# Kernel tuning notes

Measured on AMD Instinct MI355X. Metric: run time of the kernel, lower is better.

## Reference

```python
import jax, jax.numpy as jnp
import numpy as np

N, E, H = 10000, 80000, 128
NODE_DIM, EDGE_DIM, OUT_DIM, L = 7, 21, 2, 10

def _lin(k, i, o):
    s = 1.0 / np.sqrt(i)
    k1, k2 = jax.random.split(k)
    return (jax.random.uniform(k1, (i, o), jnp.float32, -s, s),
            jax.random.uniform(k2, (o,), jnp.float32, -s, s))

def _mlp_params(k, dims):
    ks = jax.random.split(k, len(dims) - 1)
    Ws, bs = [], []
    for kk, i, o in zip(ks, dims[:-1], dims[1:]):
        W, b = _lin(kk, i, o)
        Ws.append(W); bs.append(b)
    return Ws, bs

def _stack_mlps(k, dims, n):
    ks = jax.random.split(k, n)
    per = [_mlp_params(kk, dims) for kk in ks]
    Ws = [jnp.stack([p[0][j] for p in per]) for j in range(3)]
    bs = [jnp.stack([p[1][j] for p in per]) for j in range(3)]
    return Ws, bs

def mlp3(h, W1, b1, W2, b2, W3, b3):
    h = jax.nn.leaky_relu(h @ W1 + b1)  # slope 0.01 = torch LeakyReLU default
    h = jax.nn.leaky_relu(h @ W2 + b2)
    return h @ W3 + b3

def setup_inputs() -> dict:
    key = jax.random.key(0)
    ks = jax.random.split(key, 10)
    inp = {
        'x_type': jax.random.randint(ks[0], (N,), 0, 2),
        'edge_index': jax.random.randint(ks[1], (2, E), 0, N),
        'edge_attr': jax.random.normal(ks[2], (E, EDGE_DIM), jnp.float32),
        'node_dist': jax.random.uniform(ks[3], (E, 1), jnp.float32),
        'embed_w': jax.random.normal(ks[4], (2, NODE_DIM), jnp.float32),
    }
    niW, nib = _mlp_params(ks[5], [NODE_DIM, H, H, H])
    eiW, eib = _mlp_params(ks[6], [EDGE_DIM, H, H, H])
    noW, nob = _mlp_params(ks[7], [H, H, H, OUT_DIM])
    meW, meb = _stack_mlps(ks[8], [3 * H, H, H, H], L)
    mnW, mnb = _stack_mlps(ks[9], [2 * H, H, H, H], L)
    for pre, Ws, bs in [('ni', niW, nib), ('ei', eiW, eib), ('no', noW, nob),
                        ('me', meW, meb), ('mn', mnW, mnb)]:
        for j in range(3):
            inp[f'{pre}_W{j+1}'] = Ws[j]
            inp[f'{pre}_b{j+1}'] = bs[j]
    return inp

def reference(x_type, edge_index, edge_attr, node_dist, embed_w,
              ni_W1, ni_b1, ni_W2, ni_b2, ni_W3, ni_b3,
              ei_W1, ei_b1, ei_W2, ei_b2, ei_W3, ei_b3,
              no_W1, no_b1, no_W2, no_b2, no_W3, no_b3,
              me_W1, me_b1, me_W2, me_b2, me_W3, me_b3,
              mn_W1, mn_b1, mn_W2, mn_b2, mn_W3, mn_b3):
    n = x_type.shape[0]
    src, dst = edge_index[0], edge_index[1]  # PyG: j = source, i = target
    node = mlp3(embed_w[x_type], ni_W1, ni_b1, ni_W2, ni_b2, ni_W3, ni_b3)
    edge = mlp3(edge_attr, ei_W1, ei_b1, ei_W2, ei_b2, ei_W3, ei_b3)
    for i in range(L):
        # message: cat(x_i, x_j, edge_feature) -> edge MLP
        m = mlp3(jnp.concatenate([node[dst], node[src], edge], axis=-1),
                 me_W1[i], me_b1[i], me_W2[i], me_b2[i], me_W3[i], me_b3[i])
        # aggregate: scatter-sum of node_dist-weighted messages onto targets
        aggr = jax.ops.segment_sum(m * node_dist, dst, num_segments=n)
        node = node + mlp3(jnp.concatenate([node, aggr], axis=-1),
                           mn_W1[i], mn_b1[i], mn_W2[i], mn_b2[i], mn_W3[i], mn_b3[i])
        edge = edge + m
    return mlp3(node, no_W1, no_b1, no_W2, no_b2, no_W3, no_b3)
```

## Files before the change

### kernel.cpp

```cpp
#include <hip/hip_runtime.h>


#define NH  128
#define TPB 256

typedef unsigned short u16;
typedef unsigned int   u32;
using s8v = __attribute__((ext_vector_type(8))) short;
using f4v = __attribute__((ext_vector_type(4))) float;


__device__ __forceinline__ u16 bf_hi(float v) {
  u32 u = __float_as_uint(v);
  return (u16)((u + 0x7FFFu + ((u >> 16) & 1u)) >> 16);
}
__device__ __forceinline__ float bf_f(u16 h) { return __uint_as_float((u32)h << 16); }
__device__ __forceinline__ void split2(float v, u16& h, u16& l) {
  h = bf_hi(v); l = bf_hi(v - bf_f(h));
}
__device__ __forceinline__ void split8(const float* v, s8v& fh, s8v& fl) {
  union { u32 u[4]; s8v s; } H, L;
  #pragma unroll
  for (int i = 0; i < 4; ++i) {
    u16 h0, l0, h1, l1;
    split2(v[2*i], h0, l0); split2(v[2*i+1], h1, l1);
    H.u[i] = (u32)h0 | ((u32)h1 << 16);
    L.u[i] = (u32)l0 | ((u32)l1 << 16);
  }
  fh = H.s; fl = L.s;
}

__device__ __forceinline__ f4v mfma3(s8v ah, s8v al, s8v bh, s8v bl, f4v c) {
  c = __builtin_amdgcn_mfma_f32_16x16x32_bf16(ah, bh, c, 0, 0, 0);
  c = __builtin_amdgcn_mfma_f32_16x16x32_bf16(ah, bl, c, 0, 0, 0);
  c = __builtin_amdgcn_mfma_f32_16x16x32_bf16(al, bh, c, 0, 0, 0);
  return c;
}

__device__ __forceinline__ float lrelu(float v) { return v > 0.f ? v : 0.01f * v; }

__device__ __forceinline__ void pack2(f4v a, u32& w0, u32& w1, u32& v0, u32& v1) {
  u16 h[4], lo[4];
  #pragma unroll
  for (int r = 0; r < 4; ++r) { const float x = lrelu(a[r]); split2(x, h[r], lo[r]); }
  w0 = (u32)h[0]  | ((u32)h[1]  << 16); w1 = (u32)h[2]  | ((u32)h[3]  << 16);
  v0 = (u32)lo[0] | ((u32)lo[1] << 16); v1 = (u32)lo[2] | ((u32)lo[3] << 16);
}

__device__ __forceinline__ void trans_frag(f4v a0, f4v a1, int srcA, int srcB, bool sel1,
                                           s8v& fh, s8v& fl) {
  u32 h00,h01,l00,l01, h10,h11,l10,l11;
  pack2(a0, h00,h01,l00,l01);
  pack2(a1, h10,h11,l10,l11);
  union { u32 u[4]; s8v s; } H, L;
  u32 x, y;
  x = __shfl((int)h00, srcA); y = __shfl((int)h10, srcA); H.u[0] = sel1 ? y : x;
  x = __shfl((int)h01, srcA); y = __shfl((int)h11, srcA); H.u[1] = sel1 ? y : x;
  x = __shfl((int)h00, srcB); y = __shfl((int)h10, srcB); H.u[2] = sel1 ? y : x;
  x = __shfl((int)h01, srcB); y = __shfl((int)h11, srcB); H.u[3] = sel1 ? y : x;
  x = __shfl((int)l00, srcA); y = __shfl((int)l10, srcA); L.u[0] = sel1 ? y : x;
  x = __shfl((int)l01, srcA); y = __shfl((int)l11, srcA); L.u[1] = sel1 ? y : x;
  x = __shfl((int)l00, srcB); y = __shfl((int)l10, srcB); L.u[2] = sel1 ? y : x;
  x = __shfl((int)l01, srcB); y = __shfl((int)l11, srcB); L.u[3] = sel1 ? y : x;
  fh = H.s; fl = L.s;
}


__device__ __forceinline__ void stage_load(const u16* __restrict__ base, int KW, int LO,
                                           int col, int w, int l, float4 sreg[4]) {
  const int glog8 = ((l & 3) ^ ((l >> 3) & 3)) * 8;
  #pragma unroll
  for (int i = 0; i < 2; ++i) {
    const int t2 = (w * 2 + i) * 64 + l;
    const u16* gp = base + (size_t)(t2 >> 2) * KW + col + glog8;
    sreg[i*2+0] = *(const float4*)gp;
    sreg[i*2+1] = *(const float4*)(gp + LO);
  }
}
__device__ __forceinline__ void stage_write(u16* wb, int w, int l, const float4 sreg[4]) {
  #pragma unroll
  for (int i = 0; i < 2; ++i) {
    const int t2 = (w * 2 + i) * 64 + l;
    *(float4*)(wb + t2 * 8)        = sreg[i*2+0];
    *(float4*)(wb + 4096 + t2 * 8) = sreg[i*2+1];
  }
}
__device__ __forceinline__ void wfrag(const u16* panel, int tt, int c, int gsw, s8v& wh, s8v& wl) {
  const u16* p = panel + (16*tt + c) * 32 + gsw * 8;
  wh = *(const s8v*)p;
  wl = *(const s8v*)(p + 4096);
}

#define ME1_OFF 0
#define ME2_OFF 983040
#define ME3_OFF 1310720
#define MN1_OFF 1638400
#define MN2_OFF 2293760
#define MN3_OFF 2621440
#define WT_TOTAL 2949120
#define PREP_ELEMS 1474560

__global__ void __launch_bounds__(256) k_prep(
    const float* __restrict__ meW1, const float* __restrict__ meW2, const float* __restrict__ meW3,
    const float* __restrict__ mnW1, const float* __restrict__ mnW2, const float* __restrict__ mnW3,
    u16* __restrict__ wt) {
  const int id = blockIdx.x * 256 + threadIdx.x;
  if (id >= PREP_ELEMS) return;
  const int l = id / 147456;
  const int rem = id % 147456;
  const float* src; u16* dh; int K, loc;
  if (rem < 49152)       { loc = rem;          K = 384; src = meW1 + (size_t)l*49152; dh = wt + ME1_OFF + (size_t)l*98304; }
  else if (rem < 65536)  { loc = rem - 49152;  K = 128; src = meW2 + (size_t)l*16384; dh = wt + ME2_OFF + (size_t)l*32768; }
  else if (rem < 81920)  { loc = rem - 65536;  K = 128; src = meW3 + (size_t)l*16384; dh = wt + ME3_OFF + (size_t)l*32768; }
  else if (rem < 114688) { loc = rem - 81920;  K = 256; src = mnW1 + (size_t)l*32768; dh = wt + MN1_OFF + (size_t)l*65536; }
  else if (rem < 131072) { loc = rem - 114688; K = 128; src = mnW2 + (size_t)l*16384; dh = wt + MN2_OFF + (size_t)l*32768; }
  else                   { loc = rem - 131072; K = 128; src = mnW3 + (size_t)l*16384; dh = wt + MN3_OFF + (size_t)l*32768; }
  const int n = loc / K, k = loc % K;
  const float v = src[(size_t)k * NH + n];
  u16 h, lo; split2(v, h, lo);
  dh[(size_t)n * K + k] = h;
  dh[(size_t)NH * K + (size_t)n * K + k] = lo;
}


__global__ void __launch_bounds__(256) k_deg(const int* __restrict__ dst, int* __restrict__ cnt, int E) {
  const int e = blockIdx.x * 256 + threadIdx.x;
  if (e < E) atomicAdd(&cnt[dst[e]], 1);
}

__global__ void __launch_bounds__(256) k_scan(int* __restrict__ cur, int* __restrict__ off, int n, int E) {
  __shared__ int ps[256];
  const int t = threadIdx.x;
  const int chunk = (n + 255) / 256;
  const int b0 = t * chunk;
  int s = 0;
  for (int j = 0; j < chunk; ++j) { const int r = b0 + j; if (r < n) s += cur[r]; }
  ps[t] = s; __syncthreads();
  for (int d = 1; d < 256; d <<= 1) {
    const int v = (t >= d) ? ps[t - d] : 0; __syncthreads();
    ps[t] += v; __syncthreads();
  }
  int run = ps[t] - s;
  for (int j = 0; j < chunk; ++j) {
    const int r = b0 + j;
    if (r < n) { const int d = cur[r]; off[r] = run; cur[r] = run; run += d; }
  }
  if (t == 0) off[n] = E;
}

__global__ void __launch_bounds__(256) k_fill(const int* __restrict__ dst, int* __restrict__ cur,
                                              int* __restrict__ csr, int E) {
  const int e = blockIdx.x * 256 + threadIdx.x;
  if (e < E) { const int p = atomicAdd(&cur[dst[e]], 1); csr[p] = e; }
}


__device__ __forceinline__ int swzB(int c) { return c ^ ((c >> 3) & 1); }
__device__ __forceinline__ void fma8(float* a, float s, const float4 b0, const float4 b1) {
  a[0] += s * b0.x; a[1] += s * b0.y; a[2] += s * b0.z; a[3] += s * b0.w;
  a[4] += s * b1.x; a[5] += s * b1.y; a[6] += s * b1.z; a[7] += s * b1.w;
}

template<int RB>
__device__ __forceinline__ void stage_rows128(
    const float* __restrict__ src, int row_base, int nmax, float* As, int t) {
  const int c = t & 31;
  for (int e = t >> 5; e < RB; e += 8) {
    int r = row_base + e; if (r >= nmax) r = nmax - 1;
    const float4 v = reinterpret_cast<const float4*>(src + (size_t)r * NH)[c];
    reinterpret_cast<float4*>(As)[e * 32 + (c ^ ((e >> 2) & 7))] = v;
  }
}

template<int RB>
__device__ __forceinline__ void stage_smallK(
    const float* __restrict__ src, const int* __restrict__ ridx,
    int row_base, int nmax, int F, float* As, int t) {
  for (int i = t; i < RB * F; i += TPB) {
    const int e = i / F, f = i - e * F;
    int r;
    if (ridx) r = ridx[e];
    else { r = row_base + e; if (r >= nmax) r = nmax - 1; }
    As[e * NH + ((((f >> 2) ^ ((e >> 2) & 7)) << 2) | (f & 3))] = src[(size_t)r * F + f];
  }
}

template<int AR>
__device__ __forceinline__ void init_acc(const float* __restrict__ b, float acc[AR][8], int t) {
  const int o0 = (t >> 4) * 8;
  const float4 c0 = *reinterpret_cast<const float4*>(b + o0);
  const float4 c1 = *reinterpret_cast<const float4*>(b + o0 + 4);
  #pragma unroll
  for (int i = 0; i < AR; ++i) {
    acc[i][0] = c0.x; acc[i][1] = c0.y; acc[i][2] = c0.z; acc[i][3] = c0.w;
    acc[i][4] = c1.x; acc[i][5] = c1.y; acc[i][6] = c1.z; acc[i][7] = c1.w;
  }
}

template<int AR>
__device__ __forceinline__ void gemm_block(
    const float* __restrict__ W, int Kpart,
    const float* As, float* Bs, float acc[AR][8], int t) {
  const int e0  = (t & 15) * AR;
  const int g   = t >> 4;
  const int ob0 = swzB(g * 2) * 4;
  const int ob1 = swzB(g * 2 + 1) * 4;
  int sr[AR];
  #pragma unroll
  for (int i = 0; i < AR; ++i) sr[i] = ((e0 + i) >> 2) & 7;
  for (int sub = 0; sub < Kpart; sub += 32) {
    int kmax = Kpart - sub; if (kmax > 32) kmax = 32;
    __syncthreads();
    {
      const int r  = t >> 3;
      const int cb = (t & 7) * 4;
      if (r < kmax) {
        const float4* s4 = reinterpret_cast<const float4*>(W + (size_t)(sub + r) * NH) + cb;
        #pragma unroll
        for (int j = 0; j < 4; ++j)
          *reinterpret_cast<float4*>(Bs + r * NH + swzB(cb + j) * 4) = s4[j];
      }
    }
    __syncthreads();
    if (kmax == 32) {
      #pragma unroll
      for (int k4 = 0; k4 < 8; ++k4) {
        const int gch = (sub >> 2) + k4;
        float4 aa[AR];
        #pragma unroll
        for (int i = 0; i < AR; ++i)
          aa[i] = reinterpret_cast<const float4*>(As)[(e0 + i) * 32 + (gch ^ sr[i])];
        #pragma unroll
        for (int kk = 0; kk < 4; ++kk) {
          const int k = k4 * 4 + kk;
          const float4 b0 = *reinterpret_cast<const float4*>(Bs + k * NH + ob0);
          const float4 b1 = *reinterpret_cast<const float4*>(Bs + k * NH + ob1);
          #pragma unroll
          for (int i = 0; i < AR; ++i) {
            const float a = (kk == 0) ? aa[i].x : (kk == 1) ? aa[i].y : (kk == 2) ? aa[i].z : aa[i].w;
            fma8(acc[i], a, b0, b1);
          }
        }
      }
    } else {
      for (int k = 0; k < kmax; ++k) {
        const int kk = sub + k;
        const float4 b0 = *reinterpret_cast<const float4*>(Bs + k * NH + ob0);
        const float4 b1 = *reinterpret_cast<const float4*>(Bs + k * NH + ob1);
        #pragma unroll
        for (int i = 0; i < AR; ++i) {
          const float a = As[(e0 + i) * NH + ((((kk >> 2) ^ sr[i]) << 2) | (kk & 3))];
          fma8(acc[i], a, b0, b1);
        }
      }
    }
  }
}

template<int AR, bool ACT>
__device__ __forceinline__ void act_store(float* As, float acc[AR][8], int t) {
  const int e0 = (t & 15) * AR;
  const int g  = t >> 4;
  __syncthreads();
  #pragma unroll
  for (int i = 0; i < AR; ++i) {
    const int r = e0 + i;
    const int s = (r >> 2) & 7;
    float v[8];
    #pragma unroll
    for (int j = 0; j < 8; ++j) v[j] = ACT ? lrelu(acc[i][j]) : acc[i][j];
    float4 w0 = {v[0], v[1], v[2], v[3]};
    float4 w1 = {v[4], v[5], v[6], v[7]};
    reinterpret_cast<float4*>(As + r * NH)[(g * 2)     ^ s] = w0;
    reinterpret_cast<float4*>(As + r * NH)[(g * 2 + 1) ^ s] = w1;
  }
  __syncthreads();
}


__global__ void __launch_bounds__(TPB) k_enc_node(
    const int* __restrict__ xt, const float* __restrict__ embed,
    const float* __restrict__ W1, const float* __restrict__ b1,
    const float* __restrict__ W2, const float* __restrict__ b2,
    const float* __restrict__ W3, const float* __restrict__ b3,
    float* __restrict__ node, int n) {
  constexpr int RB = 32, AR = 2;
  __shared__ float As[RB * NH];
  __shared__ float Bs[32 * NH];
  __shared__ int rid[RB];
  const int t = threadIdx.x;
  const int base = blockIdx.x * RB;
  if (t < RB) { int r = base + t; if (r >= n) r = n - 1; rid[t] = xt[r]; }
  __syncthreads();
  stage_smallK<RB>(embed, rid, 0, 2, 7, As, t);
  float acc[AR][8];
  init_acc<AR>(b1, acc, t);
  gemm_block<AR>(W1, 7, As, Bs, acc, t);
  act_store<AR, true>(As, acc, t);
  init_acc<AR>(b2, acc, t);
  gemm_block<AR>(W2, NH, As, Bs, acc, t);
  act_store<AR, true>(As, acc, t);
  init_acc<AR>(b3, acc, t);
  gemm_block<AR>(W3, NH, As, Bs, acc, t);
  const int e0 = (t & 15) * AR, o0 = (t >> 4) * 8;
  #pragma unroll
  for (int i = 0; i < AR; ++i) {
    const int r = base + e0 + i;
    if (r < n) {
      float4 v0 = {acc[i][0], acc[i][1], acc[i][2], acc[i][3]};
      float4 v1 = {acc[i][4], acc[i][5], acc[i][6], acc[i][7]};
      float4* p = reinterpret_cast<float4*>(node + (size_t)r * NH + o0);
      p[0] = v0; p[1] = v1;
    }
  }
}

__global__ void __launch_bounds__(TPB) k_enc_edge(
    const float* __restrict__ ea,
    const float* __restrict__ W1, const float* __restrict__ b1,
    const float* __restrict__ W2, const float* __restrict__ b2,
    const float* __restrict__ W3, const float* __restrict__ b3,
    float* __restrict__ edge, int nE) {
  constexpr int RB = 64, AR = 4;
  __shared__ float As[RB * NH];
  __shared__ float Bs[32 * NH];
  const int t = threadIdx.x;
  const int base = blockIdx.x * RB;
  stage_smallK<RB>(ea, nullptr, base, nE, 21, As, t);
  float acc[AR][8];
  init_acc<AR>(b1, acc, t);
  gemm_block<AR>(W1, 21, As, Bs, acc, t);
  act_store<AR, true>(As, acc, t);
  init_acc<AR>(b2, acc, t);
  gemm_block<AR>(W2, NH, As, Bs, acc, t);
  act_store<AR, true>(As, acc, t);
  init_acc<AR>(b3, acc, t);
  gemm_block<AR>(W3, NH, As, Bs, acc, t);
  const int e0 = (t & 15) * AR, o0 = (t >> 4) * 8;
  #pragma unroll
  for (int i = 0; i < AR; ++i) {
    const int r = base + e0 + i;
    if (r < nE) {
      float4 v0 = {acc[i][0], acc[i][1], acc[i][2], acc[i][3]};
      float4 v1 = {acc[i][4], acc[i][5], acc[i][6], acc[i][7]};
      float4* p = reinterpret_cast<float4*>(edge + (size_t)r * NH + o0);
      p[0] = v0; p[1] = v1;
    }
  }
}

__global__ void __launch_bounds__(TPB) k_dec(
    const float* __restrict__ node,
    const float* __restrict__ W1, const float* __restrict__ b1,
    const float* __restrict__ W2, const float* __restrict__ b2,
    const float* __restrict__ W3, const float* __restrict__ b3,
    float* __restrict__ out, int n) {
  constexpr int RB = 32, AR = 2;
  __shared__ float As[RB * NH];
  __shared__ float Bs[32 * NH];
  const int t = threadIdx.x;
  const int base = blockIdx.x * RB;
  stage_rows128<RB>(node, base, n, As, t);
  float acc[AR][8];
  init_acc<AR>(b1, acc, t);
  gemm_block<AR>(W1, NH, As, Bs, acc, t);
  act_store<AR, true>(As, acc, t);
  init_acc<AR>(b2, acc, t);
  gemm_block<AR>(W2, NH, As, Bs, acc, t);
  act_store<AR, true>(As, acc, t);
  if (t < RB * 2) {
    const int e = t >> 1, oc = t & 1;
    const int r = base + e;
    if (r < n) {
      const int s = (e >> 2) & 7;
      float sum = b3[oc];
      #pragma unroll 8
      for (int k = 0; k < NH; ++k)
        sum += As[e * NH + ((((k >> 2) ^ s) << 2) | (k & 3))] * W3[k * 2 + oc];
      out[(size_t)r * 2 + oc] = sum;
    }
  }
}

__global__ void __launch_bounds__(TPB) k_msg_mm(
    const int* __restrict__ ei, const float* __restrict__ node,
    float* __restrict__ edge, const float* __restrict__ dist, float* __restrict__ mw,
    const u16* __restrict__ wt1, const u16* __restrict__ wt2, const u16* __restrict__ wt3,
    const float* __restrict__ b1, const float* __restrict__ b2, const float* __restrict__ b3,
    int E) {
  __shared__ u16 wbuf[2][8192];
  const int t = threadIdx.x, w = t >> 6, l = t & 63, c = l & 15, g = l >> 4;
  const int gsw = g ^ ((c >> 1) & 3);
  const int wbase = blockIdx.x * 128 + w * 32;
  int e0 = wbase + c, e1 = wbase + 16 + c;
  if (e0 >= E) e0 = E - 1;
  if (e1 >= E) e1 = E - 1;
  const int sj0 = ei[e0], di0 = ei[E + e0];
  const int sj1 = ei[e1], di1 = ei[E + e1];

  float4 sreg[4];
  stage_load(wt1, 384, 49152, 0, w, l, sreg);
  stage_write(wbuf[0], w, l, sreg);

  f4v acc1a[8], acc1b[8];
  #pragma unroll
  for (int tt = 0; tt < 8; ++tt) {
    const float4 bb = *(const float4*)(b1 + 16*tt + 4*g);
    acc1a[tt] = f4v{bb.x, bb.y, bb.z, bb.w};
    acc1b[tt] = acc1a[tt];
  }
  __syncthreads();

  const int srcA = ((g & 1) * 2) * 16 + c, srcB = srcA + 16;
  const bool sel1 = (g >> 1) != 0;
  int cur = 0;

  #pragma unroll
  for (int part = 0; part < 3; ++part) {
    const float* a0 = (part == 0) ? node + (size_t)di0 * NH
                    : (part == 1) ? node + (size_t)sj0 * NH
                                  : edge + (size_t)e0 * NH;
    const float* a1 = (part == 0) ? node + (size_t)di1 * NH
                    : (part == 1) ? node + (size_t)sj1 * NH
                                  : edge + (size_t)e1 * NH;
    #pragma unroll 1
    for (int kc = 0; kc < 4; ++kc) {
      if (part == 2 && kc == 3) stage_load(wt2, 128, 16384, 0, w, l, sreg);
      else                      stage_load(wt1, 384, 49152, (part*4 + kc + 1) * 32, w, l, sreg);
      s8v h0, lo0, h1, lo1;
      { float v[8];
        *(float4*)v       = *(const float4*)(a0 + kc*32 + g*8);
        *(float4*)(v + 4) = *(const float4*)(a0 + kc*32 + g*8 + 4);
        split8(v, h0, lo0);
        *(float4*)v       = *(const float4*)(a1 + kc*32 + g*8);
        *(float4*)(v + 4) = *(const float4*)(a1 + kc*32 + g*8 + 4);
        split8(v, h1, lo1); }
      const u16* panel = wbuf[cur];
      #pragma unroll
      for (int tt = 0; tt < 8; ++tt) {
        s8v wh, wl; wfrag(panel, tt, c, gsw, wh, wl);
        acc1a[tt] = mfma3(wh, wl, h0, lo0, acc1a[tt]);
        acc1b[tt] = mfma3(wh, wl, h1, lo1, acc1b[tt]);
      }
      stage_write(wbuf[cur ^ 1], w, l, sreg);
      __syncthreads();
      cur ^= 1;
    }
  }

  f4v acc2a[8], acc2b[8];
  #pragma unroll
  for (int tt = 0; tt < 8; ++tt) {
    const float4 bb = *(const float4*)(b2 + 16*tt + 4*g);
    acc2a[tt] = f4v{bb.x, bb.y, bb.z, bb.w};
    acc2b[tt] = acc2a[tt];
  }
  #pragma unroll
  for (int kc = 0; kc < 4; ++kc) {
    if (kc < 3) stage_load(wt2, 128, 16384, (kc + 1) * 32, w, l, sreg);
    else        stage_load(wt3, 128, 16384, 0, w, l, sreg);
    s8v h0, lo0, h1, lo1;
    trans_frag(acc1a[2*kc], acc1a[2*kc+1], srcA, srcB, sel1, h0, lo0);
    trans_frag(acc1b[2*kc], acc1b[2*kc+1], srcA, srcB, sel1, h1, lo1);
    const u16* panel = wbuf[cur];
    #pragma unroll
    for (int tt = 0; tt < 8; ++tt) {
      s8v wh, wl; wfrag(panel, tt, c, gsw, wh, wl);
      acc2a[tt] = mfma3(wh, wl, h0, lo0, acc2a[tt]);
      acc2b[tt] = mfma3(wh, wl, h1, lo1, acc2b[tt]);
    }
    stage_write(wbuf[cur ^ 1], w, l, sreg);
    __syncthreads();
    cur ^= 1;
  }

  f4v acc3a[8], acc3b[8];
  #pragma unroll
  for (int tt = 0; tt < 8; ++tt) {
    const float bv = b3[16*tt + c];
    acc3a[tt] = f4v{bv, bv, bv, bv};
    acc3b[tt] = acc3a[tt];
  }
  #pragma unroll
  for (int kc = 0; kc < 4; ++kc) {
    if (kc < 3) stage_load(wt3, 128, 16384, (kc + 1) * 32, w, l, sreg);
    s8v h0, lo0, h1, lo1;
    trans_frag(acc2a[2*kc], acc2a[2*kc+1], srcA, srcB, sel1, h0, lo0);
    trans_frag(acc2b[2*kc], acc2b[2*kc+1], srcA, srcB, sel1, h1, lo1);
    const u16* panel = wbuf[cur];
    #pragma unroll
    for (int tt = 0; tt < 8; ++tt) {
      s8v wh, wl; wfrag(panel, tt, c, gsw, wh, wl);
      acc3a[tt] = mfma3(h0, lo0, wh, wl, acc3a[tt]);
      acc3b[tt] = mfma3(h1, lo1, wh, wl, acc3b[tt]);
    }
    if (kc < 3) { stage_write(wbuf[cur ^ 1], w, l, sreg); __syncthreads(); cur ^= 1; }
  }

  {
    #pragma unroll
    for (int r = 0; r < 4; ++r) {
      const int e = wbase + 4*g + r;
      if (e < E) {
        const float dw = dist[e];
        #pragma unroll
        for (int tt = 0; tt < 8; ++tt) {
          const int f = 16*tt + c;
          const float m = acc3a[tt][r];
          edge[(size_t)e * NH + f] += m;
          mw[(size_t)e * NH + f] = m * dw;
        }
      }
    }
    #pragma unroll
    for (int r = 0; r < 4; ++r) {
      const int e = wbase + 16 + 4*g + r;
      if (e < E) {
        const float dw = dist[e];
        #pragma unroll
        for (int tt = 0; tt < 8; ++tt) {
          const int f = 16*tt + c;
          const float m = acc3b[tt][r];
          edge[(size_t)e * NH + f] += m;
          mw[(size_t)e * NH + f] = m * dw;
        }
      }
    }
  }
}

__global__ void __launch_bounds__(TPB) k_node_mm(
    const int* __restrict__ off, const int* __restrict__ csr, const float* __restrict__ mw,
    float* __restrict__ node,
    const u16* __restrict__ wt1, const u16* __restrict__ wt2, const u16* __restrict__ wt3,
    const float* __restrict__ b1, const float* __restrict__ b2, const float* __restrict__ b3,
    int n) {
  __shared__ float ag[64][132];
  __shared__ u16 wbuf[8192];
  const int t = threadIdx.x, w = t >> 6, l = t & 63, c = l & 15, g = l >> 4;
  const int gsw = g ^ ((c >> 1) & 3);
  const int base = blockIdx.x * 64;

  float4 sreg[4];
  stage_load(wt1, 256, 32768, 0, w, l, sreg);
  stage_write(wbuf, w, l, sreg);

  {
    const int r = t >> 2, q = t & 3;
    const int rg = base + r;
    float s[32];
    #pragma unroll
    for (int i = 0; i < 32; ++i) s[i] = 0.f;
    if (rg < n) {
      const int eb = off[rg], ee = off[rg + 1];
      for (int ii = eb; ii < ee; ++ii) {
        const float* mp = mw + (size_t)csr[ii] * NH + q * 32;
        #pragma unroll
        for (int u = 0; u < 8; ++u) {
          const float4 x = *(const float4*)(mp + u * 4);
          s[u*4+0] += x.x; s[u*4+1] += x.y; s[u*4+2] += x.z; s[u*4+3] += x.w;
        }
      }
    }
    #pragma unroll
    for (int u = 0; u < 8; ++u)
      *(float4*)&ag[r][q*32 + u*4] = float4{s[u*4+0], s[u*4+1], s[u*4+2], s[u*4+3]};
  }
  __syncthreads();

  int nB = base + 16*w + c; if (nB >= n) nB = n - 1;
  const float* aG = node + (size_t)nB * NH;
  const float* aL = &ag[16*w + c][0];

  f4v acc1[8];
  #pragma unroll
  for (int tt = 0; tt < 8; ++tt) {
    const float4 bb = *(const float4*)(b1 + 16*tt + 4*g);
    acc1[tt] = f4v{bb.x, bb.y, bb.z, bb.w};
  }
  const int srcA = ((g & 1) * 2) * 16 + c, srcB = srcA + 16;
  const bool sel1 = (g >> 1) != 0;

  #pragma unroll
  for (int part = 0; part < 2; ++part) {
    const float* ap = (part == 0) ? aG : aL;
    #pragma unroll 1
    for (int kc = 0; kc < 4; ++kc) {
      if (part == 1 && kc == 3) stage_load(wt2, 128, 16384, 0, w, l, sreg);
      else                      stage_load(wt1, 256, 32768, (part*4 + kc + 1) * 32, w, l, sreg);
      s8v h0, lo0;
      { float v[8];
        *(float4*)v       = *(const float4*)(ap + kc*32 + g*8);
        *(float4*)(v + 4) = *(const float4*)(ap + kc*32 + g*8 + 4);
        split8(v, h0, lo0); }
      #pragma unroll
      for (int tt = 0; tt < 8; ++tt) {
        s8v wh, wl; wfrag(wbuf, tt, c, gsw, wh, wl);
        acc1[tt] = mfma3(wh, wl, h0, lo0, acc1[tt]);
      }
      __syncthreads();
      stage_write(wbuf, w, l, sreg);
      __syncthreads();
    }
  }

  f4v acc2[8];
  #pragma unroll
  for (int tt = 0; tt < 8; ++tt) {
    const float4 bb = *(const float4*)(b2 + 16*tt + 4*g);
    acc2[tt] = f4v{bb.x, bb.y, bb.z, bb.w};
  }
  #pragma unroll
  for (int kc = 0; kc < 4; ++kc) {
    if (kc < 3) stage_load(wt2, 128, 16384, (kc + 1) * 32, w, l, sreg);
    else        stage_load(wt3, 128, 16384, 0, w, l, sreg);
    s8v h0, lo0;
    trans_frag(acc1[2*kc], acc1[2*kc+1], srcA, srcB, sel1, h0, lo0);
    #pragma unroll
    for (int tt = 0; tt < 8; ++tt) {
      s8v wh, wl; wfrag(wbuf, tt, c, gsw, wh, wl);
      acc2[tt] = mfma3(wh, wl, h0, lo0, acc2[tt]);
    }
    __syncthreads();
    stage_write(wbuf, w, l, sreg);
    __syncthreads();
  }

  f4v acc3[8];
  #pragma unroll
  for (int tt = 0; tt < 8; ++tt) {
    const float bv = b3[16*tt + c];
    acc3[tt] = f4v{bv, bv, bv, bv};
  }
  #pragma unroll
  for (int kc = 0; kc < 4; ++kc) {
    if (kc < 3) stage_load(wt3, 128, 16384, (kc + 1) * 32, w, l, sreg);
    s8v h0, lo0;
    trans_frag(acc2[2*kc], acc2[2*kc+1], srcA, srcB, sel1, h0, lo0);
    #pragma unroll
    for (int tt = 0; tt < 8; ++tt) {
      s8v wh, wl; wfrag(wbuf, tt, c, gsw, wh, wl);
      acc3[tt] = mfma3(h0, lo0, wh, wl, acc3[tt]);
    }
    if (kc < 3) { __syncthreads(); stage_write(wbuf, w, l, sreg); __syncthreads(); }
  }

  #pragma unroll
  for (int r = 0; r < 4; ++r) {
    const int e = base + 16*w + 4*g + r;
    if (e < n) {
      #pragma unroll
      for (int tt = 0; tt < 8; ++tt) {
        const int f = 16*tt + c;
        node[(size_t)e * NH + f] += acc3[tt][r];
      }
    }
  }
}


extern "C" void kernel_launch(void* const* d_in, const int* in_sizes, int n_in,
                              void* d_out, int out_size, void* d_ws, size_t ws_size,
                              hipStream_t stream) {
  const int n = in_sizes[0];
  const int E = in_sizes[3];
  const int* xt      = (const int*)d_in[0];
  const int* ei      = (const int*)d_in[1];
  const float* eattr = (const float*)d_in[2];
  const float* dist  = (const float*)d_in[3];
  const float* embed = (const float*)d_in[4];
  const float* niW1 = (const float*)d_in[5];  const float* nib1 = (const float*)d_in[6];
  const float* niW2 = (const float*)d_in[7];  const float* nib2 = (const float*)d_in[8];
  const float* niW3 = (const float*)d_in[9];  const float* nib3 = (const float*)d_in[10];
  const float* eiW1 = (const float*)d_in[11]; const float* eib1 = (const float*)d_in[12];
  const float* eiW2 = (const float*)d_in[13]; const float* eib2 = (const float*)d_in[14];
  const float* eiW3 = (const float*)d_in[15]; const float* eib3 = (const float*)d_in[16];
  const float* noW1 = (const float*)d_in[17]; const float* nob1 = (const float*)d_in[18];
  const float* noW2 = (const float*)d_in[19]; const float* nob2 = (const float*)d_in[20];
  const float* noW3 = (const float*)d_in[21]; const float* nob3 = (const float*)d_in[22];
  const float* meW1 = (const float*)d_in[23]; const float* meb1 = (const float*)d_in[24];
  const float* meW2 = (const float*)d_in[25]; const float* meb2 = (const float*)d_in[26];
  const float* meW3 = (const float*)d_in[27]; const float* meb3 = (const float*)d_in[28];
  const float* mnW1 = (const float*)d_in[29]; const float* mnb1 = (const float*)d_in[30];
  const float* mnW2 = (const float*)d_in[31]; const float* mnb2 = (const float*)d_in[32];
  const float* mnW3 = (const float*)d_in[33]; const float* mnb3 = (const float*)d_in[34];

  float* out = (float*)d_out;
  const size_t fn = (size_t)n * NH;
  const size_t fe = (size_t)E * NH;

  float* node = (float*)d_ws;
  float* edge = node + fn;
  float* mw   = edge + fe;
  u16*   wt   = (u16*)(mw + fe);
  int*   off  = (int*)(wt + WT_TOTAL);
  int*   cur  = off + (n + 1);
  int*   csr  = cur + n;

  const int nb32   = (n + 31) / 32;
  const int nb64n  = (n + 63) / 64;
  const int nb64e  = (E + 63) / 64;
  const int nb128e = (E + 127) / 128;

  k_prep<<<(PREP_ELEMS + 255) / 256, 256, 0, stream>>>(meW1, meW2, meW3, mnW1, mnW2, mnW3, wt);

  hipMemsetAsync(cur, 0, (size_t)n * sizeof(int), stream);
  k_deg <<<(E + 255) / 256, 256, 0, stream>>>(ei + E, cur, E);
  k_scan<<<1, 256, 0, stream>>>(cur, off, n, E);
  k_fill<<<(E + 255) / 256, 256, 0, stream>>>(ei + E, cur, csr, E);

  k_enc_node<<<nb32,  TPB, 0, stream>>>(xt, embed, niW1, nib1, niW2, nib2, niW3, nib3, node, n);
  k_enc_edge<<<nb64e, TPB, 0, stream>>>(eattr, eiW1, eib1, eiW2, eib2, eiW3, eib3, edge, E);

  for (int l = 0; l < 10; ++l) {
    k_msg_mm<<<nb128e, TPB, 0, stream>>>(ei, node, edge, dist, mw,
        wt + ME1_OFF + (size_t)l * 98304,
        wt + ME2_OFF + (size_t)l * 32768,
        wt + ME3_OFF + (size_t)l * 32768,
        meb1 + (size_t)l * NH, meb2 + (size_t)l * NH, meb3 + (size_t)l * NH, E);
    k_node_mm<<<nb64n, TPB, 0, stream>>>(off, csr, mw, node,
        wt + MN1_OFF + (size_t)l * 65536,
        wt + MN2_OFF + (size_t)l * 32768,
        wt + MN3_OFF + (size_t)l * 32768,
        mnb1 + (size_t)l * NH, mnb2 + (size_t)l * NH, mnb3 + (size_t)l * NH, n);
  }

  k_dec<<<nb32, TPB, 0, stream>>>(node, noW1, nob1, noW2, nob2, noW3, nob3, out, n);
}
```

Measured before the change: 1.750 ms.

## Halve block size, prefetch activation chunks, and raise MFMA wave priority

Both per-layer kernels move from 256-thread to 128-thread blocks, so each block covers 64 edges or 32 nodes and twice as many blocks launch. The weight-staging helpers now load twice as many vectors per thread to fill the same panel. The activation chunk for the next K-step is loaded one step ahead in registers so its global latency overlaps the current MFMAs. s_setprio is raised around the MFMA loops to favour waves issuing matrix work. In exchange, each block re-stages the full weight panels for fewer rows, which adds L2 traffic, and register pressure rises.

```diff
diff --git a/kernel.cpp b/kernel.cpp
--- a/kernel.cpp
+++ b/kernel.cpp
@@ -67,20 +67,20 @@
 
 
 __device__ __forceinline__ void stage_load(const u16* __restrict__ base, int KW, int LO,
-                                           int col, int w, int l, float4 sreg[4]) {
-  const int glog8 = ((l & 3) ^ ((l >> 3) & 3)) * 8;
-  #pragma unroll
-  for (int i = 0; i < 2; ++i) {
-    const int t2 = (w * 2 + i) * 64 + l;
+                                           int col, int t, float4 sreg[8]) {
+  const int glog8 = ((t & 3) ^ ((t >> 3) & 3)) * 8;
+  #pragma unroll
+  for (int i = 0; i < 4; ++i) {
+    const int t2 = i * 128 + t;
     const u16* gp = base + (size_t)(t2 >> 2) * KW + col + glog8;
     sreg[i*2+0] = *(const float4*)gp;
     sreg[i*2+1] = *(const float4*)(gp + LO);
   }
 }
-__device__ __forceinline__ void stage_write(u16* wb, int w, int l, const float4 sreg[4]) {
-  #pragma unroll
-  for (int i = 0; i < 2; ++i) {
-    const int t2 = (w * 2 + i) * 64 + l;
+__device__ __forceinline__ void stage_write(u16* wb, int t, const float4 sreg[8]) {
+  #pragma unroll
+  for (int i = 0; i < 4; ++i) {
+    const int t2 = i * 128 + t;
     *(float4*)(wb + t2 * 8)        = sreg[i*2+0];
     *(float4*)(wb + 4096 + t2 * 8) = sreg[i*2+1];
   }
@@ -382,7 +382,7 @@
   }
 }
 
-__global__ void __launch_bounds__(TPB) k_msg_mm(
+__global__ void __launch_bounds__(128) k_msg_mm(
     const int* __restrict__ ei, const float* __restrict__ node,
     float* __restrict__ edge, const float* __restrict__ dist, float* __restrict__ mw,
     const u16* __restrict__ wt1, const u16* __restrict__ wt2, const u16* __restrict__ wt3,
@@ -391,16 +391,23 @@
   __shared__ u16 wbuf[2][8192];
   const int t = threadIdx.x, w = t >> 6, l = t & 63, c = l & 15, g = l >> 4;
   const int gsw = g ^ ((c >> 1) & 3);
-  const int wbase = blockIdx.x * 128 + w * 32;
+  const int wbase = blockIdx.x * 64 + w * 32;
   int e0 = wbase + c, e1 = wbase + 16 + c;
   if (e0 >= E) e0 = E - 1;
   if (e1 >= E) e1 = E - 1;
   const int sj0 = ei[e0], di0 = ei[E + e0];
   const int sj1 = ei[e1], di1 = ei[E + e1];
 
-  float4 sreg[4];
-  stage_load(wt1, 384, 49152, 0, w, l, sreg);
-  stage_write(wbuf[0], w, l, sreg);
+  const float* ap0[3] = { node + (size_t)di0 * NH, node + (size_t)sj0 * NH, edge + (size_t)e0 * NH };
+  const float* ap1[3] = { node + (size_t)di1 * NH, node + (size_t)sj1 * NH, edge + (size_t)e1 * NH };
+
+  float4 sreg[8];
+  stage_load(wt1, 384, 49152, 0, t, sreg);
+  float4 aC0 = *(const float4*)(ap0[0] + g*8);
+  float4 aC1 = *(const float4*)(ap0[0] + g*8 + 4);
+  float4 aC2 = *(const float4*)(ap1[0] + g*8);
+  float4 aC3 = *(const float4*)(ap1[0] + g*8 + 4);
+  stage_write(wbuf[0], t, sreg);
 
   f4v acc1a[8], acc1b[8];
   #pragma unroll
@@ -416,36 +423,34 @@
   int cur = 0;
 
   #pragma unroll
-  for (int part = 0; part < 3; ++part) {
-    const float* a0 = (part == 0) ? node + (size_t)di0 * NH
-                    : (part == 1) ? node + (size_t)sj0 * NH
-                                  : edge + (size_t)e0 * NH;
-    const float* a1 = (part == 0) ? node + (size_t)di1 * NH
-                    : (part == 1) ? node + (size_t)sj1 * NH
-                                  : edge + (size_t)e1 * NH;
-    #pragma unroll 1
-    for (int kc = 0; kc < 4; ++kc) {
-      if (part == 2 && kc == 3) stage_load(wt2, 128, 16384, 0, w, l, sreg);
-      else                      stage_load(wt1, 384, 49152, (part*4 + kc + 1) * 32, w, l, sreg);
-      s8v h0, lo0, h1, lo1;
-      { float v[8];
-        *(float4*)v       = *(const float4*)(a0 + kc*32 + g*8);
-        *(float4*)(v + 4) = *(const float4*)(a0 + kc*32 + g*8 + 4);
-        split8(v, h0, lo0);
-        *(float4*)v       = *(const float4*)(a1 + kc*32 + g*8);
-        *(float4*)(v + 4) = *(const float4*)(a1 + kc*32 + g*8 + 4);
-        split8(v, h1, lo1); }
-      const u16* panel = wbuf[cur];
-      #pragma unroll
-      for (int tt = 0; tt < 8; ++tt) {
-        s8v wh, wl; wfrag(panel, tt, c, gsw, wh, wl);
-        acc1a[tt] = mfma3(wh, wl, h0, lo0, acc1a[tt]);
-        acc1b[tt] = mfma3(wh, wl, h1, lo1, acc1b[tt]);
-      }
-      stage_write(wbuf[cur ^ 1], w, l, sreg);
-      __syncthreads();
-      cur ^= 1;
-    }
+  for (int p = 0; p < 12; ++p) {
+    float4 aN0, aN1, aN2, aN3;
+    if (p < 11) {
+      const int pt = (p + 1) >> 2, kn = (p + 1) & 3;
+      aN0 = *(const float4*)(ap0[pt] + kn*32 + g*8);
+      aN1 = *(const float4*)(ap0[pt] + kn*32 + g*8 + 4);
+      aN2 = *(const float4*)(ap1[pt] + kn*32 + g*8);
+      aN3 = *(const float4*)(ap1[pt] + kn*32 + g*8 + 4);
+    }
+    if (p < 11) stage_load(wt1, 384, 49152, (p + 1) * 32, t, sreg);
+    else        stage_load(wt2, 128, 16384, 0, t, sreg);
+    s8v h0, lo0, h1, lo1;
+    { float v[8];
+      *(float4*)v = aC0; *(float4*)(v + 4) = aC1; split8(v, h0, lo0);
+      *(float4*)v = aC2; *(float4*)(v + 4) = aC3; split8(v, h1, lo1); }
+    const u16* panel = wbuf[cur];
+    __builtin_amdgcn_s_setprio(1);
+    #pragma unroll
+    for (int tt = 0; tt < 8; ++tt) {
+      s8v wh, wl; wfrag(panel, tt, c, gsw, wh, wl);
+      acc1a[tt] = mfma3(wh, wl, h0, lo0, acc1a[tt]);
+      acc1b[tt] = mfma3(wh, wl, h1, lo1, acc1b[tt]);
+    }
+    __builtin_amdgcn_s_setprio(0);
+    stage_write(wbuf[cur ^ 1], t, sreg);
+    __syncthreads();
+    cur ^= 1;
+    if (p < 11) { aC0 = aN0; aC1 = aN1; aC2 = aN2; aC3 = aN3; }
   }
 
   f4v acc2a[8], acc2b[8];
@@ -457,19 +462,21 @@
   }
   #pragma unroll
   for (int kc = 0; kc < 4; ++kc) {
-    if (kc < 3) stage_load(wt2, 128, 16384, (kc + 1) * 32, w, l, sreg);
-    else        stage_load(wt3, 128, 16384, 0, w, l, sreg);
+    if (kc < 3) stage_load(wt2, 128, 16384, (kc + 1) * 32, t, sreg);
+    else        stage_load(wt3, 128, 16384, 0, t, sreg);
     s8v h0, lo0, h1, lo1;
     trans_frag(acc1a[2*kc], acc1a[2*kc+1], srcA, srcB, sel1, h0, lo0);
     trans_frag(acc1b[2*kc], acc1b[2*kc+1], srcA, srcB, sel1, h1, lo1);
     const u16* panel = wbuf[cur];
+    __builtin_amdgcn_s_setprio(1);
     #pragma unroll
     for (int tt = 0; tt < 8; ++tt) {
       s8v wh, wl; wfrag(panel, tt, c, gsw, wh, wl);
       acc2a[tt] = mfma3(wh, wl, h0, lo0, acc2a[tt]);
       acc2b[tt] = mfma3(wh, wl, h1, lo1, acc2b[tt]);
     }
-    stage_write(wbuf[cur ^ 1], w, l, sreg);
+    __builtin_amdgcn_s_setprio(0);
+    stage_write(wbuf[cur ^ 1], t, sreg);
     __syncthreads();
     cur ^= 1;
   }
@@ -483,67 +490,72 @@
   }
   #pragma unroll
   for (int kc = 0; kc < 4; ++kc) {
-    if (kc < 3) stage_load(wt3, 128, 16384, (kc + 1) * 32, w, l, sreg);
+    if (kc < 3) stage_load(wt3, 128, 16384, (kc + 1) * 32, t, sreg);
     s8v h0, lo0, h1, lo1;
     trans_frag(acc2a[2*kc], acc2a[2*kc+1], srcA, srcB, sel1, h0, lo0);
     trans_frag(acc2b[2*kc], acc2b[2*kc+1], srcA, srcB, sel1, h1, lo1);
     const u16* panel = wbuf[cur];
+    __builtin_amdgcn_s_setprio(1);
     #pragma unroll
     for (int tt = 0; tt < 8; ++tt) {
       s8v wh, wl; wfrag(panel, tt, c, gsw, wh, wl);
       acc3a[tt] = mfma3(h0, lo0, wh, wl, acc3a[tt]);
       acc3b[tt] = mfma3(h1, lo1, wh, wl, acc3b[tt]);
     }
-    if (kc < 3) { stage_write(wbuf[cur ^ 1], w, l, sreg); __syncthreads(); cur ^= 1; }
-  }
-
-  {
-    #pragma unroll
-    for (int r = 0; r < 4; ++r) {
-      const int e = wbase + 4*g + r;
-      if (e < E) {
-        const float dw = dist[e];
-        #pragma unroll
-        for (int tt = 0; tt < 8; ++tt) {
-          const int f = 16*tt + c;
-          const float m = acc3a[tt][r];
-          edge[(size_t)e * NH + f] += m;
-          mw[(size_t)e * NH + f] = m * dw;
-        }
+    __builtin_amdgcn_s_setprio(0);
+    if (kc < 3) { stage_write(wbuf[cur ^ 1], t, sreg); __syncthreads(); cur ^= 1; }
+  }
+
+  #pragma unroll
+  for (int r = 0; r < 4; ++r) {
+    const int e = wbase + 4*g + r;
+    if (e < E) {
+      const float dw = dist[e];
+      #pragma unroll
+      for (int tt = 0; tt < 8; ++tt) {
+        const int f = 16*tt + c;
+        const float m = acc3a[tt][r];
+        edge[(size_t)e * NH + f] += m;
+        mw[(size_t)e * NH + f] = m * dw;
       }
     }
-    #pragma unroll
-    for (int r = 0; r < 4; ++r) {
-      const int e = wbase + 16 + 4*g + r;
-      if (e < E) {
-        const float dw = dist[e];
-        #pragma unroll
-        for (int tt = 0; tt < 8; ++tt) {
-          const int f = 16*tt + c;
-          const float m = acc3b[tt][r];
-          edge[(size_t)e * NH + f] += m;
-          mw[(size_t)e * NH + f] = m * dw;
-        }
+  }
+  #pragma unroll
+  for (int r = 0; r < 4; ++r) {
+    const int e = wbase + 16 + 4*g + r;
+    if (e < E) {
+      const float dw = dist[e];
+      #pragma unroll
+      for (int tt = 0; tt < 8; ++tt) {
+        const int f = 16*tt + c;
+        const float m = acc3b[tt][r];
+        edge[(size_t)e * NH + f] += m;
+        mw[(size_t)e * NH + f] = m * dw;
       }
     }
   }
 }
 
-__global__ void __launch_bounds__(TPB) k_node_mm(
+__global__ void __launch_bounds__(128) k_node_mm(
     const int* __restrict__ off, const int* __restrict__ csr, const float* __restrict__ mw,
     float* __restrict__ node,
     const u16* __restrict__ wt1, const u16* __restrict__ wt2, const u16* __restrict__ wt3,
     const float* __restrict__ b1, const float* __restrict__ b2, const float* __restrict__ b3,
     int n) {
-  __shared__ float ag[64][132];
+  __shared__ float ag[32][132];
   __shared__ u16 wbuf[8192];
   const int t = threadIdx.x, w = t >> 6, l = t & 63, c = l & 15, g = l >> 4;
   const int gsw = g ^ ((c >> 1) & 3);
-  const int base = blockIdx.x * 64;
-
-  float4 sreg[4];
-  stage_load(wt1, 256, 32768, 0, w, l, sreg);
-  stage_write(wbuf, w, l, sreg);
+  const int base = blockIdx.x * 32;
+
+  float4 sreg[8];
+  stage_load(wt1, 256, 32768, 0, t, sreg);
+
+  int nB = base + 16*w + c; if (nB >= n) nB = n - 1;
+  const float* aG = node + (size_t)nB * NH;
+  float4 aC0 = *(const float4*)(aG + g*8);
+  float4 aC1 = *(const float4*)(aG + g*8 + 4);
+  stage_write(wbuf, t, sreg);
 
   {
     const int r = t >> 2, q = t & 3;
@@ -568,8 +580,6 @@
   }
   __syncthreads();
 
-  int nB = base + 16*w + c; if (nB >= n) nB = n - 1;
-  const float* aG = node + (size_t)nB * NH;
   const float* aL = &ag[16*w + c][0];
 
   f4v acc1[8];
@@ -582,26 +592,35 @@
   const bool sel1 = (g >> 1) != 0;
 
   #pragma unroll
-  for (int part = 0; part < 2; ++part) {
-    const float* ap = (part == 0) ? aG : aL;
-    #pragma unroll 1
-    for (int kc = 0; kc < 4; ++kc) {
-      if (part == 1 && kc == 3) stage_load(wt2, 128, 16384, 0, w, l, sreg);
-      else                      stage_load(wt1, 256, 32768, (part*4 + kc + 1) * 32, w, l, sreg);
-      s8v h0, lo0;
-      { float v[8];
-        *(float4*)v       = *(const float4*)(ap + kc*32 + g*8);
-        *(float4*)(v + 4) = *(const float4*)(ap + kc*32 + g*8 + 4);
-        split8(v, h0, lo0); }
-      #pragma unroll
-      for (int tt = 0; tt < 8; ++tt) {
-        s8v wh, wl; wfrag(wbuf, tt, c, gsw, wh, wl);
-        acc1[tt] = mfma3(wh, wl, h0, lo0, acc1[tt]);
-      }
-      __syncthreads();
-      stage_write(wbuf, w, l, sreg);
-      __syncthreads();
-    }
+  for (int p = 0; p < 8; ++p) {
+    const int part = p >> 2, kc = p & 3;
+    float4 aN0, aN1;
+    if (p < 3) {
+      aN0 = *(const float4*)(aG + (kc + 1)*32 + g*8);
+      aN1 = *(const float4*)(aG + (kc + 1)*32 + g*8 + 4);
+    }
+    if (p < 7) stage_load(wt1, 256, 32768, (p + 1) * 32, t, sreg);
+    else       stage_load(wt2, 128, 16384, 0, t, sreg);
+    s8v h0, lo0;
+    if (part == 0) {
+      float v[8]; *(float4*)v = aC0; *(float4*)(v + 4) = aC1; split8(v, h0, lo0);
+    } else {
+      float v[8];
+      *(float4*)v       = *(const float4*)(aL + kc*32 + g*8);
+      *(float4*)(v + 4) = *(const float4*)(aL + kc*32 + g*8 + 4);
+      split8(v, h0, lo0);
+    }
+    __builtin_amdgcn_s_setprio(1);
+    #pragma unroll
+    for (int tt = 0; tt < 8; ++tt) {
+      s8v wh, wl; wfrag(wbuf, tt, c, gsw, wh, wl);
+      acc1[tt] = mfma3(wh, wl, h0, lo0, acc1[tt]);
+    }
+    __builtin_amdgcn_s_setprio(0);
+    __syncthreads();
+    stage_write(wbuf, t, sreg);
+    __syncthreads();
+    if (p < 3) { aC0 = aN0; aC1 = aN1; }
   }
 
   f4v acc2[8];
@@ -612,17 +631,19 @@
   }
   #pragma unroll
   for (int kc = 0; kc < 4; ++kc) {
-    if (kc < 3) stage_load(wt2, 128, 16384, (kc + 1) * 32, w, l, sreg);
-    else        stage_load(wt3, 128, 16384, 0, w, l, sreg);
+    if (kc < 3) stage_load(wt2, 128, 16384, (kc + 1) * 32, t, sreg);
+    else        stage_load(wt3, 128, 16384, 0, t, sreg);
     s8v h0, lo0;
     trans_frag(acc1[2*kc], acc1[2*kc+1], srcA, srcB, sel1, h0, lo0);
+    __builtin_amdgcn_s_setprio(1);
     #pragma unroll
     for (int tt = 0; tt < 8; ++tt) {
       s8v wh, wl; wfrag(wbuf, tt, c, gsw, wh, wl);
       acc2[tt] = mfma3(wh, wl, h0, lo0, acc2[tt]);
     }
+    __builtin_amdgcn_s_setprio(0);
     __syncthreads();
-    stage_write(wbuf, w, l, sreg);
+    stage_write(wbuf, t, sreg);
     __syncthreads();
   }
 
@@ -634,15 +655,17 @@
   }
   #pragma unroll
   for (int kc = 0; kc < 4; ++kc) {
-    if (kc < 3) stage_load(wt3, 128, 16384, (kc + 1) * 32, w, l, sreg);
+    if (kc < 3) stage_load(wt3, 128, 16384, (kc + 1) * 32, t, sreg);
     s8v h0, lo0;
     trans_frag(acc2[2*kc], acc2[2*kc+1], srcA, srcB, sel1, h0, lo0);
+    __builtin_amdgcn_s_setprio(1);
     #pragma unroll
     for (int tt = 0; tt < 8; ++tt) {
       s8v wh, wl; wfrag(wbuf, tt, c, gsw, wh, wl);
       acc3[tt] = mfma3(h0, lo0, wh, wl, acc3[tt]);
     }
-    if (kc < 3) { __syncthreads(); stage_write(wbuf, w, l, sreg); __syncthreads(); }
+    __builtin_amdgcn_s_setprio(0);
+    if (kc < 3) { __syncthreads(); stage_write(wbuf, t, sreg); __syncthreads(); }
   }
 
   #pragma unroll
@@ -697,10 +720,8 @@
   int*   cur  = off + (n + 1);
   int*   csr  = cur + n;
 
-  const int nb32   = (n + 31) / 32;
-  const int nb64n  = (n + 63) / 64;
-  const int nb64e  = (E + 63) / 64;
-  const int nb128e = (E + 127) / 128;
+  const int nb32  = (n + 31) / 32;
+  const int nb64e = (E + 63) / 64;
 
   k_prep<<<(PREP_ELEMS + 255) / 256, 256, 0, stream>>>(meW1, meW2, meW3, mnW1, mnW2, mnW3, wt);
 
@@ -713,12 +734,12 @@
   k_enc_edge<<<nb64e, TPB, 0, stream>>>(eattr, eiW1, eib1, eiW2, eib2, eiW3, eib3, edge, E);
 
   for (int l = 0; l < 10; ++l) {
-    k_msg_mm<<<nb128e, TPB, 0, stream>>>(ei, node, edge, dist, mw,
+    k_msg_mm<<<nb64e, 128, 0, stream>>>(ei, node, edge, dist, mw,
         wt + ME1_OFF + (size_t)l * 98304,
         wt + ME2_OFF + (size_t)l * 32768,
         wt + ME3_OFF + (size_t)l * 32768,
         meb1 + (size_t)l * NH, meb2 + (size_t)l * NH, meb3 + (size_t)l * NH, E);
-    k_node_mm<<<nb64n, TPB, 0, stream>>>(off, csr, mw, node,
+    k_node_mm<<<nb32, 128, 0, stream>>>(off, csr, mw, node,
         wt + MN1_OFF + (size_t)l * 65536,
         wt + MN2_OFF + (size_t)l * 32768,
         wt + MN3_OFF + (size_t)l * 32768,
```

After: 2.227 ms. +27.3%, slower.
